# Kernel tuning notes

Hardware: AMD Instinct MI355X
Metric: run time of the kernel (lower is better)

The kernel has to match this reference:

```python
import jax, jax.numpy as jnp
import numpy as np

# Geometry constants matching PointLoss.__init__ defaults
FOV_H = 360.0   # horizontal FOV (deg)
FOV_VU = 3.0    # upper vertical FOV (deg)
DH = 0.5        # delta_h
DV = 0.5        # delta_v
PROJ_H = 52     # int(26 / 0.5)
PROJ_W = 720    # int(360 / 0.5)
THETAC = 0.5    # confidence threshold
LAMDA = 1.0     # fov-loss weight
ANGRATE = 1.0   # anglelossrate
EPS = 1e-8


def setup_inputs() -> dict:
    key = jax.random.key(0)
    ks = jax.random.split(key, 10)
    B, H, W = 64, PROJ_H, PROJ_W
    return {
        "vertexmap_proj": jax.random.normal(ks[0], (B, H, W, 3), jnp.float32),
        "normalmap_proj": jax.random.normal(ks[1], (B, H, W, 3), jnp.float32),
        "uncertainty": jax.random.uniform(ks[2], (B, H, W), jnp.float32),
        "now_normalmap": jax.random.normal(ks[3], (B, H, W, 3), jnp.float32),
        "now_confidencemap": jax.random.uniform(ks[4], (B, H, W), jnp.float32),
        "last_normalmap": jax.random.normal(ks[5], (B, H, W, 3), jnp.float32),
        "last_vertexmap": jax.random.normal(ks[6], (B, H, W, 3), jnp.float32),
        "sx": jnp.zeros((1,), jnp.float32),
        "sq": jnp.zeros((1,), jnp.float32),
        "now_maskmap": jax.random.randint(ks[7], (B, H, W), 0, 2, jnp.int32),
        "last_maskmap": jax.random.randint(ks[8], (B, H, W), 0, 2, jnp.int32),
    }


def _gather_proj(m, flat_idx, B, H, W):
    """Gather pixels of m [B,H,W,(C)] at flat index [B,H,W] -> same shape as m."""
    if m.ndim == 3:
        mf = m.reshape(B, H * W)
        return jnp.take_along_axis(mf, flat_idx.reshape(B, H * W), axis=1).reshape(B, H, W)
    C = m.shape[-1]
    mf = m.reshape(B, H * W, C)
    idx = jnp.broadcast_to(flat_idx.reshape(B, H * W, 1), (B, H * W, C))
    return jnp.take_along_axis(mf, idx, axis=1).reshape(B, H, W, C)


def reference(vertexmap_proj, normalmap_proj, uncertainty, now_normalmap,
              now_confidencemap, last_normalmap, last_vertexmap, sx, sq,
              now_maskmap, last_maskmap):
    B, H, W, _ = vertexmap_proj.shape
    v = vertexmap_proj

    # mask of valid current pixels: maskmap > 0 and normal non-zero
    mask0 = (now_maskmap > 0) & (jnp.sum(jnp.abs(now_normalmap), -1) != 0)

    # spherical re-projection (movegrid=True)
    depth = jnp.sqrt(jnp.sum(v * v, -1) + EPS)
    yaw = jnp.arctan2(v[..., 1], v[..., 0]) * (180.0 / np.pi)
    pitch = jnp.arcsin(jnp.clip(v[..., 2] / depth, -1.0, 1.0)) * (180.0 / np.pi)
    proj_x = (FOV_H / 2 - yaw) / DH
    proj_y = (FOV_VU - pitch) / DV

    # fov loss = masked mse(proj, clamp(proj)) (F.mse_loss default mean)
    m0 = mask0.astype(v.dtype)
    n0 = jnp.maximum(jnp.sum(m0), 1.0)
    fovloss = (jnp.sum(m0 * (proj_x - jnp.clip(proj_x, 0, W - 1)) ** 2)
               + jnp.sum(m0 * (proj_y - jnp.clip(proj_y, 0, H - 1)) ** 2)) / n0

    prx = jnp.round(proj_x)
    pry = jnp.round(proj_y)
    inb = (prx >= 0) & (prx < W) & (pry >= 0) & (pry < H)
    prxi = jnp.clip(prx, 0, W - 1).astype(jnp.int32)
    pryi = jnp.clip(pry, 0, H - 1).astype(jnp.int32)
    flat = pryi * W + prxi  # [B,H,W]

    nl = _gather_proj(last_normalmap, flat, B, H, W)   # last normal at projected pixel
    vl = _gather_proj(last_vertexmap, flat, B, H, W)   # last vertex at projected pixel
    lm = _gather_proj(last_maskmap, flat, B, H, W)

    lastmask = (lm > 0) & (jnp.sum(jnp.abs(nl), -1) != 0)
    mask = mask0 & inb & lastmask & (now_confidencemap >= THETAC)
    m = mask.astype(v.dtype)
    n = jnp.maximum(jnp.sum(m), 1.0)

    # point-to-plane ICP residual, uncertainty-weighted L1
    r = jnp.sum(nl * (v - vl), -1)
    icploss = jnp.sum(m * uncertainty * jnp.abs(r)) / n

    # angular loss: 1 - |cos(angle between normals)|
    nn = normalmap_proj
    cosang = jnp.abs(jnp.sum(nl * nn, -1)) / jnp.sqrt(
        jnp.sum(nl * nl, -1) * jnp.sum(nn * nn, -1) + EPS)
    angloss = jnp.sum(m * uncertainty * (1.0 - cosang)) / n

    sx0, sq0 = sx[0], sq[0]
    total = (jnp.exp(-sx0) * icploss + sx0
             + ANGRATE * jnp.exp(-sq0) * angloss + sq0
             + LAMDA * fovloss)
    return total
```

## Files before the change

### kernel.cpp

```cpp
#include <hip/hip_runtime.h>
#include <math.h>


namespace {
constexpr int B_ = 64, H_ = 52, W_ = 720;
constexpr int HW_ = H_ * W_;
constexpr int NPIX = B_ * HW_;
constexpr int NT = 256;
constexpr int NB = 2048;
constexpr int STRIDE = NB * NT;
constexpr int NI = 5;
constexpr float EPSF = 1e-8f;
constexpr float RAD2DEG = 57.29577951308232f;
}

__device__ __forceinline__ float atan_poly01(float z) {
    const float z2 = z * z;
    float r = fmaf(z2, -0.0117212f, 0.0526526f);
    r = fmaf(z2, r, -0.1164329f);
    r = fmaf(z2, r,  0.1935435f);
    r = fmaf(z2, r, -0.3326235f);
    r = fmaf(z2, r,  0.9999773f);
    return r * z;
}

__device__ __forceinline__ float atan2_fast(float y, float x) {
    const float ax = fabsf(x), ay = fabsf(y);
    const float mx = fmaxf(ax, ay), mn = fminf(ax, ay);
    const float z = mn * __builtin_amdgcn_rcpf(fmaxf(mx, 1e-37f));
    float a = atan_poly01(z);
    if (ay > ax) a = 1.5707964f - a;
    if (x < 0.0f) a = 3.1415927f - a;
    return copysignf(a, y);
}

__device__ __forceinline__ float asin_core(float x) {
    const float x2 = x * x;
    float r = fmaf(x2, 0.03038196f, 0.04464286f);
    r = fmaf(x2, r, 0.075f);
    r = fmaf(x2, r, 0.16666667f);
    return fmaf(x * x2, r, x);
}

__device__ __forceinline__ float asin_fast(float q) {
    const float a = fabsf(q);
    const float r1 = asin_core(a);
    const float s = sqrtf(fmaxf(0.5f * (1.0f - a), 0.0f));
    const float r2 = 1.5707964f - 2.0f * asin_core(s);
    const float r = (a > 0.5f) ? r2 : r1;
    return copysignf(r, q);
}

__global__ __launch_bounds__(NT, 4) void pointloss_main(
    const float* __restrict__ v,
    const float* __restrict__ nrm,
    const float* __restrict__ unc,
    const float* __restrict__ nown,
    const float* __restrict__ conf,
    const float* __restrict__ lastn,
    const float* __restrict__ lastv,
    const int*   __restrict__ nowm,
    const int*   __restrict__ lastm,
    float* __restrict__ partials)
{
    const int base = blockIdx.x * NT + threadIdx.x;

    int   pp[NI];
    bool  pv[NI];
    #pragma unroll
    for (int j = 0; j < NI; ++j) {
        const int pj = base + j * STRIDE;
        pv[j] = (pj < NPIX);
        pp[j] = pv[j] ? pj : base;
    }

    float vx[NI], vy[NI], vz[NI], ax[NI], ay[NI], az[NI], cf[NI], uv[NI];
    int mi[NI];
    #pragma unroll
    for (int j = 0; j < NI; ++j) {
        const int p = pp[j];
        vx[j] = v[3*p];    vy[j] = v[3*p+1];    vz[j] = v[3*p+2];
        ax[j] = nown[3*p]; ay[j] = nown[3*p+1]; az[j] = nown[3*p+2];
        mi[j] = nowm[p];   cf[j] = conf[p];     uv[j] = unc[p];
    }

    float px[NI], py[NI];
    bool  m0[NI], pred[NI];
    int   gi[NI];
    #pragma unroll
    for (int j = 0; j < NI; ++j) {
        m0[j] = pv[j] && (mi[j] > 0) &&
                ((fabsf(ax[j]) + fabsf(ay[j]) + fabsf(az[j])) != 0.0f);
        const float d2 = vx[j]*vx[j] + vy[j]*vy[j] + vz[j]*vz[j] + EPSF;
        const float q  = fminf(fmaxf(vz[j] * __builtin_amdgcn_rsqf(d2), -1.f), 1.f);
        const float yaw   = atan2_fast(vy[j], vx[j]) * RAD2DEG;
        const float pitch = asin_fast(q) * RAD2DEG;
        px[j] = (180.0f - yaw) * 2.0f;
        py[j] = (3.0f - pitch) * 2.0f;
        const float prx = rintf(px[j]), pry = rintf(py[j]);
        const bool inb = (prx >= 0.f) && (prx < 720.f) &&
                         (pry >= 0.f) && (pry < 52.f);
        pred[j] = m0[j] && inb && (cf[j] >= 0.5f);
        gi[j] = pred[j] ? ((pp[j] / HW_) * HW_ + (int)pry * W_ + (int)prx)
                        : pp[j];
    }

    float lx[NI], ly[NI], lz[NI], wx[NI], wy[NI], wz[NI];
    float nx[NI], ny[NI], nz[NI];
    int   lmv[NI];
    #pragma unroll
    for (int j = 0; j < NI; ++j) {
        if (pred[j]) {
            const int g = gi[j], p = pp[j];
            lx[j] = lastn[3*g]; ly[j] = lastn[3*g+1]; lz[j] = lastn[3*g+2];
            lmv[j] = lastm[g];
            wx[j] = lastv[3*g]; wy[j] = lastv[3*g+1]; wz[j] = lastv[3*g+2];
            nx[j] = nrm[3*p];   ny[j] = nrm[3*p+1];   nz[j] = nrm[3*p+2];
        }
    }

    float s_m0 = 0.f, s_fov = 0.f, s_m = 0.f, s_icp = 0.f, s_ang = 0.f;
    #pragma unroll
    for (int j = 0; j < NI; ++j) {
        if (m0[j]) {
            const float dx = px[j] - fminf(fmaxf(px[j], 0.f), 719.0f);
            const float dy = py[j] - fminf(fmaxf(py[j], 0.f), 51.0f);
            s_m0 += 1.0f;
            s_fov += dx*dx + dy*dy;
        }
    }

    #pragma unroll
    for (int j = 0; j < NI; ++j) {
        if (pred[j] && (lmv[j] > 0) &&
            ((fabsf(lx[j]) + fabsf(ly[j]) + fabsf(lz[j])) != 0.f)) {
            const float r  = lx[j]*(vx[j]-wx[j]) + ly[j]*(vy[j]-wy[j])
                           + lz[j]*(vz[j]-wz[j]);
            const float dt = lx[j]*nx[j] + ly[j]*ny[j] + lz[j]*nz[j];
            const float den = (lx[j]*lx[j] + ly[j]*ly[j] + lz[j]*lz[j]) *
                              (nx[j]*nx[j] + ny[j]*ny[j] + nz[j]*nz[j]) + EPSF;
            const float cosang = fabsf(dt) * __builtin_amdgcn_rsqf(den);
            s_m   += 1.0f;
            s_icp += uv[j] * fabsf(r);
            s_ang += uv[j] * (1.0f - cosang);
        }
    }

    #pragma unroll
    for (int off = 32; off > 0; off >>= 1) {
        s_m0  += __shfl_down(s_m0,  off);
        s_fov += __shfl_down(s_fov, off);
        s_m   += __shfl_down(s_m,   off);
        s_icp += __shfl_down(s_icp, off);
        s_ang += __shfl_down(s_ang, off);
    }
    __shared__ float red[NT / 64][5];
    const int lane = threadIdx.x & 63;
    const int wv   = threadIdx.x >> 6;
    if (lane == 0) {
        red[wv][0] = s_m0;  red[wv][1] = s_fov; red[wv][2] = s_m;
        red[wv][3] = s_icp; red[wv][4] = s_ang;
    }
    __syncthreads();
    if (threadIdx.x == 0) {
        float tt[5] = {0.f, 0.f, 0.f, 0.f, 0.f};
        for (int w2 = 0; w2 < NT / 64; ++w2)
            for (int c = 0; c < 5; ++c) tt[c] += red[w2][c];
        float* o = partials + blockIdx.x * 5;
        for (int c = 0; c < 5; ++c) o[c] = tt[c];
    }
}

__global__ __launch_bounds__(256) void pointloss_finalize(
    const float* __restrict__ partials,
    const float* __restrict__ sx,
    const float* __restrict__ sq,
    float* __restrict__ out)
{
    double a0 = 0, a1 = 0, a2 = 0, a3 = 0, a4 = 0;
    for (int i = threadIdx.x; i < NB; i += 256) {
        const float* pq = partials + i * 5;
        a0 += (double)pq[0]; a1 += (double)pq[1]; a2 += (double)pq[2];
        a3 += (double)pq[3]; a4 += (double)pq[4];
    }
    #pragma unroll
    for (int off = 32; off > 0; off >>= 1) {
        a0 += __shfl_down(a0, off);
        a1 += __shfl_down(a1, off);
        a2 += __shfl_down(a2, off);
        a3 += __shfl_down(a3, off);
        a4 += __shfl_down(a4, off);
    }
    __shared__ double red[4][5];
    const int lane = threadIdx.x & 63;
    const int wv   = threadIdx.x >> 6;
    if (lane == 0) {
        red[wv][0] = a0; red[wv][1] = a1; red[wv][2] = a2;
        red[wv][3] = a3; red[wv][4] = a4;
    }
    __syncthreads();
    if (threadIdx.x == 0) {
        double t[5] = {0, 0, 0, 0, 0};
        for (int w2 = 0; w2 < 4; ++w2)
            for (int c = 0; c < 5; ++c) t[c] += red[w2][c];
        const double n0 = fmax(t[0], 1.0);
        const double n  = fmax(t[2], 1.0);
        const double sx0 = (double)sx[0], sq0 = (double)sq[0];
        const double total = exp(-sx0) * (t[3] / n) + sx0
                           + exp(-sq0) * (t[4] / n) + sq0
                           + t[1] / n0;
        out[0] = (float)total;
    }
}

extern "C" void kernel_launch(void* const* d_in, const int* in_sizes, int n_in,
                              void* d_out, int out_size, void* d_ws, size_t ws_size,
                              hipStream_t stream) {
    const float* v     = (const float*)d_in[0];
    const float* nrm   = (const float*)d_in[1];
    const float* unc   = (const float*)d_in[2];
    const float* nown  = (const float*)d_in[3];
    const float* conf  = (const float*)d_in[4];
    const float* lastn = (const float*)d_in[5];
    const float* lastv = (const float*)d_in[6];
    const float* sx    = (const float*)d_in[7];
    const float* sq    = (const float*)d_in[8];
    const int*   nowm  = (const int*)d_in[9];
    const int*   lastm = (const int*)d_in[10];

    float* partials = (float*)d_ws;

    pointloss_main<<<NB, NT, 0, stream>>>(
        v, nrm, unc, nown, conf, lastn, lastv, nowm, lastm, partials);
    pointloss_finalize<<<1, 256, 0, stream>>>(partials, sx, sq, (float*)d_out);
}
```

Measured before the change: 196.4 us.

## Switch to one pixel per thread with full grid and SoA partials

Replaces the grid-stride kernel, which handled five pixels per thread over 2048 blocks, with one thread per pixel over NPIX/256 blocks. The normal map is now loaded unconditionally and the gather is done inline under the predicate. Partials are stored column-major, and the finalize kernel is widened to 1024 threads to reduce the much larger partial count. The intent is to raise occupancy and simplify scheduling, at the cost of many more blocks and more partials to reduce.

Measured after the change: 200.0 us. No clear change (+1.8%).

```diff
diff --git a/kernel.cpp b/kernel.cpp
--- a/kernel.cpp
+++ b/kernel.cpp
@@ -7,9 +7,7 @@
 constexpr int HW_ = H_ * W_;
 constexpr int NPIX = B_ * HW_;
 constexpr int NT = 256;
-constexpr int NB = 2048;
-constexpr int STRIDE = NB * NT;
-constexpr int NI = 5;
+constexpr int NB = NPIX / NT;
 constexpr float EPSF = 1e-8f;
 constexpr float RAD2DEG = 57.29577951308232f;
 }
@@ -51,7 +49,7 @@
     return copysignf(r, q);
 }
 
-__global__ __launch_bounds__(NT, 4) void pointloss_main(
+__global__ __launch_bounds__(NT) void pointloss_main(
     const float* __restrict__ v,
     const float* __restrict__ nrm,
     const float* __restrict__ unc,
@@ -63,86 +61,51 @@
     const int*   __restrict__ lastm,
     float* __restrict__ partials)
 {
-    const int base = blockIdx.x * NT + threadIdx.x;
+    const int p = blockIdx.x * NT + threadIdx.x;
 
-    int   pp[NI];
-    bool  pv[NI];
-    #pragma unroll
-    for (int j = 0; j < NI; ++j) {
-        const int pj = base + j * STRIDE;
-        pv[j] = (pj < NPIX);
-        pp[j] = pv[j] ? pj : base;
+    const float vx = v[3*p],    vy = v[3*p+1],    vz = v[3*p+2];
+    const float ax = nown[3*p], ay = nown[3*p+1], az = nown[3*p+2];
+    const int   mi = nowm[p];
+    const float cf = conf[p];
+    const float uv = unc[p];
+    const float nx = nrm[3*p],  ny = nrm[3*p+1],  nz = nrm[3*p+2];
+
+    const bool mask0 = (mi > 0) &&
+                       ((fabsf(ax) + fabsf(ay) + fabsf(az)) != 0.0f);
+
+    const float d2 = vx*vx + vy*vy + vz*vz + EPSF;
+    const float q  = fminf(fmaxf(vz * __builtin_amdgcn_rsqf(d2), -1.f), 1.f);
+    const float yaw   = atan2_fast(vy, vx) * RAD2DEG;
+    const float pitch = asin_fast(q) * RAD2DEG;
+    const float px = (180.0f - yaw) * 2.0f;
+    const float py = (3.0f - pitch) * 2.0f;
+
+    float s_m0 = 0.f, s_fov = 0.f, s_m = 0.f, s_icp = 0.f, s_ang = 0.f;
+    if (mask0) {
+        const float dx = px - fminf(fmaxf(px, 0.f), 719.0f);
+        const float dy = py - fminf(fmaxf(py, 0.f), 51.0f);
+        s_m0 = 1.0f;
+        s_fov = dx*dx + dy*dy;
     }
 
-    float vx[NI], vy[NI], vz[NI], ax[NI], ay[NI], az[NI], cf[NI], uv[NI];
-    int mi[NI];
-    #pragma unroll
-    for (int j = 0; j < NI; ++j) {
-        const int p = pp[j];
-        vx[j] = v[3*p];    vy[j] = v[3*p+1];    vz[j] = v[3*p+2];
-        ax[j] = nown[3*p]; ay[j] = nown[3*p+1]; az[j] = nown[3*p+2];
-        mi[j] = nowm[p];   cf[j] = conf[p];     uv[j] = unc[p];
-    }
+    const float prx = rintf(px), pry = rintf(py);
+    const bool inb = (prx >= 0.f) && (prx < 720.f) &&
+                     (pry >= 0.f) && (pry < 52.f);
 
-    float px[NI], py[NI];
-    bool  m0[NI], pred[NI];
-    int   gi[NI];
-    #pragma unroll
-    for (int j = 0; j < NI; ++j) {
-        m0[j] = pv[j] && (mi[j] > 0) &&
-                ((fabsf(ax[j]) + fabsf(ay[j]) + fabsf(az[j])) != 0.0f);
-        const float d2 = vx[j]*vx[j] + vy[j]*vy[j] + vz[j]*vz[j] + EPSF;
-        const float q  = fminf(fmaxf(vz[j] * __builtin_amdgcn_rsqf(d2), -1.f), 1.f);
-        const float yaw   = atan2_fast(vy[j], vx[j]) * RAD2DEG;
-        const float pitch = asin_fast(q) * RAD2DEG;
-        px[j] = (180.0f - yaw) * 2.0f;
-        py[j] = (3.0f - pitch) * 2.0f;
-        const float prx = rintf(px[j]), pry = rintf(py[j]);
-        const bool inb = (prx >= 0.f) && (prx < 720.f) &&
-                         (pry >= 0.f) && (pry < 52.f);
-        pred[j] = m0[j] && inb && (cf[j] >= 0.5f);
-        gi[j] = pred[j] ? ((pp[j] / HW_) * HW_ + (int)pry * W_ + (int)prx)
-                        : pp[j];
-    }
-
-    float lx[NI], ly[NI], lz[NI], wx[NI], wy[NI], wz[NI];
-    float nx[NI], ny[NI], nz[NI];
-    int   lmv[NI];
-    #pragma unroll
-    for (int j = 0; j < NI; ++j) {
-        if (pred[j]) {
-            const int g = gi[j], p = pp[j];
-            lx[j] = lastn[3*g]; ly[j] = lastn[3*g+1]; lz[j] = lastn[3*g+2];
-            lmv[j] = lastm[g];
-            wx[j] = lastv[3*g]; wy[j] = lastv[3*g+1]; wz[j] = lastv[3*g+2];
-            nx[j] = nrm[3*p];   ny[j] = nrm[3*p+1];   nz[j] = nrm[3*p+2];
-        }
-    }
-
-    float s_m0 = 0.f, s_fov = 0.f, s_m = 0.f, s_icp = 0.f, s_ang = 0.f;
-    #pragma unroll
-    for (int j = 0; j < NI; ++j) {
-        if (m0[j]) {
-            const float dx = px[j] - fminf(fmaxf(px[j], 0.f), 719.0f);
-            const float dy = py[j] - fminf(fmaxf(py[j], 0.f), 51.0f);
-            s_m0 += 1.0f;
-            s_fov += dx*dx + dy*dy;
-        }
-    }
-
-    #pragma unroll
-    for (int j = 0; j < NI; ++j) {
-        if (pred[j] && (lmv[j] > 0) &&
-            ((fabsf(lx[j]) + fabsf(ly[j]) + fabsf(lz[j])) != 0.f)) {
-            const float r  = lx[j]*(vx[j]-wx[j]) + ly[j]*(vy[j]-wy[j])
-                           + lz[j]*(vz[j]-wz[j]);
-            const float dt = lx[j]*nx[j] + ly[j]*ny[j] + lz[j]*nz[j];
-            const float den = (lx[j]*lx[j] + ly[j]*ly[j] + lz[j]*lz[j]) *
-                              (nx[j]*nx[j] + ny[j]*ny[j] + nz[j]*nz[j]) + EPSF;
+    if (mask0 && inb && (cf >= 0.5f)) {
+        const int gi = p - (p % HW_) + (int)pry * W_ + (int)prx;
+        const float lx = lastn[3*gi], ly = lastn[3*gi+1], lz = lastn[3*gi+2];
+        const int   lmv = lastm[gi];
+        const float wx = lastv[3*gi], wy = lastv[3*gi+1], wz = lastv[3*gi+2];
+        if ((lmv > 0) && ((fabsf(lx) + fabsf(ly) + fabsf(lz)) != 0.f)) {
+            const float r  = lx*(vx-wx) + ly*(vy-wy) + lz*(vz-wz);
+            const float dt = lx*nx + ly*ny + lz*nz;
+            const float den = (lx*lx + ly*ly + lz*lz) *
+                              (nx*nx + ny*ny + nz*nz) + EPSF;
             const float cosang = fabsf(dt) * __builtin_amdgcn_rsqf(den);
-            s_m   += 1.0f;
-            s_icp += uv[j] * fabsf(r);
-            s_ang += uv[j] * (1.0f - cosang);
+            s_m   = 1.0f;
+            s_icp = uv * fabsf(r);
+            s_ang = uv * (1.0f - cosang);
         }
     }
 
@@ -166,42 +129,39 @@
         float tt[5] = {0.f, 0.f, 0.f, 0.f, 0.f};
         for (int w2 = 0; w2 < NT / 64; ++w2)
             for (int c = 0; c < 5; ++c) tt[c] += red[w2][c];
-        float* o = partials + blockIdx.x * 5;
-        for (int c = 0; c < 5; ++c) o[c] = tt[c];
+        #pragma unroll
+        for (int c = 0; c < 5; ++c)
+            partials[c * NB + blockIdx.x] = tt[c];
     }
 }
 
-__global__ __launch_bounds__(256) void pointloss_finalize(
+__global__ __launch_bounds__(1024) void pointloss_finalize(
     const float* __restrict__ partials,
     const float* __restrict__ sx,
     const float* __restrict__ sq,
     float* __restrict__ out)
 {
-    double a0 = 0, a1 = 0, a2 = 0, a3 = 0, a4 = 0;
-    for (int i = threadIdx.x; i < NB; i += 256) {
-        const float* pq = partials + i * 5;
-        a0 += (double)pq[0]; a1 += (double)pq[1]; a2 += (double)pq[2];
-        a3 += (double)pq[3]; a4 += (double)pq[4];
+    double a[5] = {0, 0, 0, 0, 0};
+    for (int i = threadIdx.x; i < NB; i += 1024) {
+        #pragma unroll
+        for (int c = 0; c < 5; ++c) a[c] += (double)partials[c * NB + i];
     }
     #pragma unroll
     for (int off = 32; off > 0; off >>= 1) {
-        a0 += __shfl_down(a0, off);
-        a1 += __shfl_down(a1, off);
-        a2 += __shfl_down(a2, off);
-        a3 += __shfl_down(a3, off);
-        a4 += __shfl_down(a4, off);
+        #pragma unroll
+        for (int c = 0; c < 5; ++c) a[c] += __shfl_down(a[c], off);
     }
-    __shared__ double red[4][5];
+    __shared__ double red[16][5];
     const int lane = threadIdx.x & 63;
     const int wv   = threadIdx.x >> 6;
     if (lane == 0) {
-        red[wv][0] = a0; red[wv][1] = a1; red[wv][2] = a2;
-        red[wv][3] = a3; red[wv][4] = a4;
+        #pragma unroll
+        for (int c = 0; c < 5; ++c) red[wv][c] = a[c];
     }
     __syncthreads();
     if (threadIdx.x == 0) {
         double t[5] = {0, 0, 0, 0, 0};
-        for (int w2 = 0; w2 < 4; ++w2)
+        for (int w2 = 0; w2 < 16; ++w2)
             for (int c = 0; c < 5; ++c) t[c] += red[w2][c];
         const double n0 = fmax(t[0], 1.0);
         const double n  = fmax(t[2], 1.0);
@@ -232,5 +192,5 @@
 
     pointloss_main<<<NB, NT, 0, stream>>>(
         v, nrm, unc, nown, conf, lastn, lastv, nowm, lastm, partials);
-    pointloss_finalize<<<1, 256, 0, stream>>>(partials, sx, sq, (float*)d_out);
+    pointloss_finalize<<<1, 1024, 0, stream>>>(partials, sx, sq, (float*)d_out);
 }
```
